# Kernel tuning notes

Hardware: AMD Instinct MI355X
Metric: run time of the kernel (lower is better)

Reference implementation:

```python
import jax, jax.numpy as jnp
import numpy as np

KH, KW, PAD, DIL, STRIDE = 3, 3, 1, 1, 1


def _conv2d(x, w):
    # plain dense conv, NCHW / OIHW, stride 1, pad 1
    return jax.lax.conv_general_dilated(
        x, w, window_strides=(STRIDE, STRIDE),
        padding=[(PAD, PAD), (PAD, PAD)],
        rhs_dilation=(DIL, DIL),
        dimension_numbers=('NCHW', 'OIHW', 'NCHW'))


def _deform_patches(x, offset):
    """Bilinear-sample deformable patches.
    x: [B,C,H,W], offset: [B,2K,Ho,Wo] with per-tap (dy,dx).
    Returns [B,C,K,Ho,Wo]."""
    B, C, H, W = x.shape
    Ho, Wo = offset.shape[2], offset.shape[3]
    K = KH * KW
    off = offset.reshape(B, K, 2, Ho, Wo)

    ky = jnp.repeat(jnp.arange(KH), KW)            # [K]
    kx = jnp.tile(jnp.arange(KW), KH)              # [K]
    base_y = (jnp.arange(Ho) * STRIDE - PAD)[None, :, None] + (DIL * ky)[:, None, None]  # [K,Ho,1]
    base_x = (jnp.arange(Wo) * STRIDE - PAD)[None, None, :] + (DIL * kx)[:, None, None]  # [K,1,Wo]

    sy = base_y[None].astype(x.dtype) + off[:, :, 0]   # [B,K,Ho,Wo]
    sx = base_x[None].astype(x.dtype) + off[:, :, 1]

    y0 = jnp.floor(sy); x0 = jnp.floor(sx)
    ly = sy - y0;       lx = sx - x0
    y0i = y0.astype(jnp.int32); x0i = x0.astype(jnp.int32)

    x_flat = x.reshape(B, C, H * W)

    def corner(yi, xi, wgt):
        valid = (yi >= 0) & (yi < H) & (xi >= 0) & (xi < W)   # zero padding outside
        idx = (jnp.clip(yi, 0, H - 1) * W + jnp.clip(xi, 0, W - 1))  # [B,K,Ho,Wo]
        gath = jax.vmap(lambda img, i: img[:, i.reshape(-1)])(x_flat, idx)  # [B,C,K*Ho*Wo]
        gath = gath.reshape(B, C, K, Ho, Wo)
        return gath * (wgt * valid.astype(x.dtype))[:, None]

    p = corner(y0i,     x0i,     (1 - ly) * (1 - lx))
    p = p + corner(y0i,     x0i + 1, (1 - ly) * lx)
    p = p + corner(y0i + 1, x0i,     ly * (1 - lx))
    p = p + corner(y0i + 1, x0i + 1, ly * lx)
    return p  # [B,C,K,Ho,Wo]


def setup_inputs() -> dict:
    key = jax.random.key(0)
    k1, k2, k3 = jax.random.split(key, 3)
    B, C, H, W = 8, 256, 64, 64
    Cout = 256
    x = jax.random.normal(k1, (B, C, H, W), dtype=jnp.float32)
    offset_w = jax.random.normal(k2, (2 * KH * KW, C, KH, KW), dtype=jnp.float32) * 0.02
    deform_w = jax.random.normal(k3, (Cout, C, KH, KW), dtype=jnp.float32) * 0.02
    return {"x": x, "offset_w": offset_w, "deform_w": deform_w}


def reference(x, offset_w, deform_w):
    # 1) offset-predicting conv
    offset = _conv2d(x, offset_w)                    # [B,2K,H,W]
    # 2) deformable conv = bilinear gather + contraction over (Cin, K)
    patches = _deform_patches(x, offset)             # [B,C,K,H,W]
    Cout = deform_w.shape[0]
    wk = deform_w.reshape(Cout, deform_w.shape[1], KH * KW)
    y = jnp.einsum('bckhw,ock->bohw', patches, wk)   # [B,Cout,H,W]
    # 3) avg + std channel attention (torch.std default: unbiased, ddof=1)
    avg = jnp.mean(y, axis=(2, 3), keepdims=True)
    std = jnp.std(y, axis=(2, 3), keepdims=True, ddof=1)
    attn = jax.nn.sigmoid(avg + std)
    return y * attn
```

## Files before the change

### kernel.cpp

```cpp
#include <hip/hip_runtime.h>
#include <hip/hip_bf16.h>
#include <math.h>

#define C_IN 256
#define H_   64
#define W_   64
#define B_   8
#define COUT 256
#define HW   (H_*W_)

typedef float f32x4 __attribute__((ext_vector_type(4)));
typedef short short8 __attribute__((ext_vector_type(8)));

static __device__ __forceinline__ int pack_bf16x2(float a, float b) {
    __hip_bfloat162 h = __float22bfloat162_rn(make_float2(a, b));
    union { __hip_bfloat162 h; int i; } u; u.h = h;
    return u.i;
}

static __device__ __forceinline__ void unpk(int v, float& lo, float& hi) {
    union { int i; float f; } a, b;
    a.i = v << 16;
    b.i = v & 0xffff0000;
    lo = a.f; hi = b.f;
}

__global__ __launch_bounds__(256) void prep_weights_kernel(
    const float* __restrict__ ow, const float* __restrict__ dw,
    short* __restrict__ wR, short* __restrict__ wO)
{
    int blk = blockIdx.x;
    int k   = blk / 288;
    int row = blk % 288;
    int c   = threadIdx.x;
    int cblk = c >> 6, ks = (c >> 5) & 1, q = (c >> 3) & 3, ce = c & 7;
    union { float f; unsigned u; } a;
    if (row < 256) {
        int o = row;
        a.f = dw[(size_t)o * 2304 + c * 9 + k];
        unsigned r = (a.u + 0x7fffu + ((a.u >> 16) & 1u)) >> 16;
        size_t idx = (size_t)(k * 8 + cblk * 2 + ks) * 8192
                   + (size_t)(o >> 4) * 512 + q * 128 + (o & 15) * 8 + ce;
        wR[idx] = (short)r;
    } else {
        int o = row - 256;
        a.f = (o < 18) ? ow[(size_t)o * 2304 + c * 9 + k] : 0.f;
        unsigned r = (a.u + 0x7fffu + ((a.u >> 16) & 1u)) >> 16;
        size_t idx = (size_t)(k * 8 + cblk * 2 + ks) * 1024
                   + (size_t)(o >> 4) * 512 + q * 128 + (o & 15) * 8 + ce;
        wO[idx] = (short)r;
    }
}

__global__ __launch_bounds__(256) void transpose_x_kernel(
    const float* __restrict__ x, unsigned short* __restrict__ xT)
{
    __shared__ float tile[64][257];
    const int tid = threadIdx.x;
    const int b = blockIdx.x >> 6, h = blockIdx.x & 63;
    const float* xb = x + ((size_t)b << 20) + h * 64;

#pragma unroll
    for (int pass = 0; pass < 16; ++pass) {
        int c  = pass * 16 + (tid >> 4);
        int w0 = (tid & 15) * 4;
        float4 v = *(const float4*)(xb + (size_t)c * 4096 + w0);
        tile[w0][c] = v.x; tile[w0 + 1][c] = v.y;
        tile[w0 + 2][c] = v.z; tile[w0 + 3][c] = v.w;
    }
    __syncthreads();

    int4* ob = (int4*)(xT + ((size_t)blockIdx.x << 14));
#pragma unroll
    for (int pass = 0; pass < 8; ++pass) {
        int idx = pass * 256 + tid;
        int w = idx >> 5, ch8 = idx & 31;
        const float* tr = &tile[w][ch8 * 8];
        int4 pk;
        pk.x = pack_bf16x2(tr[0], tr[1]);
        pk.y = pack_bf16x2(tr[2], tr[3]);
        pk.z = pack_bf16x2(tr[4], tr[5]);
        pk.w = pack_bf16x2(tr[6], tr[7]);
        ob[idx] = pk;
    }
}

__global__ __launch_bounds__(256, 2) void offset_mfma_kernel(
    const unsigned short* __restrict__ xT, const short* __restrict__ wO,
    float* __restrict__ offs)
{
    __shared__ int4 bT[2][64 * 8];

    const int tid = threadIdx.x;
    const int b   = blockIdx.x & 7;
    const int ho  = blockIdx.x >> 3;

    const int px = tid >> 2;
    const int cg = tid & 3;
    const int wv = tid >> 6;
    const int ln = tid & 63;
    const int lo = ln & 15;
    const int quad = ln >> 4;
    const int pxl = wv * 16 + lo;

    f32x4 acc[2];
    acc[0] = (f32x4){0.f, 0.f, 0.f, 0.f};
    acc[1] = (f32x4){0.f, 0.f, 0.f, 0.f};

    const unsigned short* xbb = xT + ((size_t)b << 20);
    const int4 zero4 = {0, 0, 0, 0};

    auto stageB = [&](int s, int buf) {
        int k = s >> 2, c0 = (s & 3) << 6;
        int yy = ho + k / 3 - 1;
        int xx = px + k % 3 - 1;
        bool valid = (yy >= 0) & (yy < 64) & (xx >= 0) & (xx < 64);
        int yc = min(max(yy, 0), 63), xc = min(max(xx, 0), 63);
        const int4* src = (const int4*)(xbb + (((size_t)yc * 64 + xc) << 8) + c0 + cg * 16);
        int4 p0 = valid ? src[0] : zero4;
        int4 p1 = valid ? src[1] : zero4;
        bT[buf][px * 8 + ((2 * cg)     ^ (px & 7))] = p0;
        bT[buf][px * 8 + ((2 * cg + 1) ^ (px & 7))] = p1;
    };

    stageB(0, 0);
    __syncthreads();

    for (int s = 0; s < 36; ++s) {
        const int cur = s & 1;
        if (s < 35) stageB(s + 1, cur ^ 1);

        const int k = s >> 2;
        const short* wkb = wO + (size_t)(k * 8 + (s & 3) * 2) * 1024 + ln * 8;
#pragma unroll
        for (int ks = 0; ks < 2; ++ks) {
            int ch = ks * 4 + quad;
            short8 bfr = *(const short8*)&bT[cur][pxl * 8 + (ch ^ (pxl & 7))];
#pragma unroll
            for (int t = 0; t < 2; ++t) {
                short8 afr = *(const short8*)(wkb + ks * 1024 + t * 512);
                acc[t] = __builtin_amdgcn_mfma_f32_16x16x32_bf16(afr, bfr, acc[t], 0, 0, 0);
            }
        }
        __syncthreads();
    }

#pragma unroll
    for (int t = 0; t < 2; ++t) {
#pragma unroll
        for (int r = 0; r < 4; ++r) {
            int o = t * 16 + quad * 4 + r;
            if (o < 18)
                offs[((size_t)b * 18 + o) * HW + ho * 64 + wv * 16 + lo] = acc[t][r];
        }
    }
}

__global__ __launch_bounds__(256, 4) void deform_mfma_kernel(
    const unsigned short* __restrict__ xT, const float* __restrict__ offs,
    const short* __restrict__ wR, float* __restrict__ y,
    float* __restrict__ sum_, float* __restrict__ sumsq_)
{
    __shared__ int4   meta_i[288];
    __shared__ float4 meta_w[288];
    __shared__ int4   bT[2][32 * 8];

    const int tid = threadIdx.x;
    const int b   = blockIdx.x & 7;
    const int ho  = (blockIdx.x >> 3) & 63;
    const int xh  = blockIdx.x >> 9;
    const int px0 = xh * 32;

    for (int e = tid; e < 288; e += 256) {
        int kk  = e >> 5;
        int pxe = px0 + (e & 31);
        float dy = offs[((size_t)b * 18 + 2 * kk)     * HW + ho * W_ + pxe];
        float dx = offs[((size_t)b * 18 + 2 * kk + 1) * HW + ho * W_ + pxe];
        float sy = (float)(ho - 1 + kk / 3) + dy;
        float sx = (float)(pxe - 1 + kk % 3) + dx;
        float y0f = floorf(sy), x0f = floorf(sx);
        float ly = sy - y0f, lx = sx - x0f;
        int y0 = (int)y0f, x0 = (int)x0f;
        int y1 = y0 + 1, x1 = x0 + 1;
        float wy0 = 1.f - ly, wx0 = 1.f - lx;
        bool vy0 = (y0 >= 0) & (y0 < H_), vy1 = (y1 >= 0) & (y1 < H_);
        bool vx0 = (x0 >= 0) & (x0 < W_), vx1 = (x1 >= 0) & (x1 < W_);
        int cy0 = min(max(y0, 0), H_ - 1), cy1 = min(max(y1, 0), H_ - 1);
        int cx0 = min(max(x0, 0), W_ - 1), cx1 = min(max(x1, 0), W_ - 1);
        int4 ii; float4 ww;
        ii.x = cy0 * W_ + cx0;  ww.x = wy0 * wx0 * ((vy0 & vx0) ? 1.f : 0.f);
        ii.y = cy0 * W_ + cx1;  ww.y = wy0 * lx  * ((vy0 & vx1) ? 1.f : 0.f);
        ii.z = cy1 * W_ + cx0;  ww.z = ly  * wx0 * ((vy1 & vx0) ? 1.f : 0.f);
        ii.w = cy1 * W_ + cx1;  ww.w = ly  * lx  * ((vy1 & vx1) ? 1.f : 0.f);
        meta_i[e] = ii;
        meta_w[e] = ww;
    }

    const int px = tid >> 3;
    const int cg = tid & 7;
    const int wv = tid >> 6;
    const int ln = tid & 63;
    const int lo = ln & 15;
    const int quad = ln >> 4;

    f32x4 acc[4][2];
#pragma unroll
    for (int t = 0; t < 4; ++t)
#pragma unroll
        for (int p = 0; p < 2; ++p)
            acc[t][p] = (f32x4){0.f, 0.f, 0.f, 0.f};

    const unsigned short* xbb = xT + ((size_t)b << 20) + cg * 8;

    int4 gA, gB, gC, gD;
    float4 ww;
    auto blend = [&](int av, int bv, int cv, int dv) -> int {
        float alo, ahi, blo, bhi, clo, chi, dlo, dhi;
        unpk(av, alo, ahi); unpk(bv, blo, bhi);
        unpk(cv, clo, chi); unpk(dv, dlo, dhi);
        float vlo = ww.x * alo + ww.y * blo + ww.z * clo + ww.w * dlo;
        float vhi = ww.x * ahi + ww.y * bhi + ww.z * chi + ww.w * dhi;
        return pack_bf16x2(vlo, vhi);
    };

    __syncthreads();

    {
        int4 ii = meta_i[px];
        ww = meta_w[px];
        gA = *(const int4*)(xbb + ((size_t)ii.x << 8));
        gB = *(const int4*)(xbb + ((size_t)ii.y << 8));
        gC = *(const int4*)(xbb + ((size_t)ii.z << 8));
        gD = *(const int4*)(xbb + ((size_t)ii.w << 8));
        int4 o0;
        o0.x = blend(gA.x, gB.x, gC.x, gD.x);
        o0.y = blend(gA.y, gB.y, gC.y, gD.y);
        o0.z = blend(gA.z, gB.z, gC.z, gD.z);
        o0.w = blend(gA.w, gB.w, gC.w, gD.w);
        bT[0][px * 8 + (cg ^ (px & 7))] = o0;
    }
    __syncthreads();

    for (int s = 0; s < 36; ++s) {
        const int cur = s & 1;
        const bool hasNext = (s < 35);

        if (hasNext) {
            int sn = s + 1;
            int kn = sn >> 2, cn = (sn & 3) << 6;
            int4 ii = meta_i[kn * 32 + px];
            ww = meta_w[kn * 32 + px];
            const unsigned short* xc = xbb + cn;
            gA = *(const int4*)(xc + ((size_t)ii.x << 8));
            gB = *(const int4*)(xc + ((size_t)ii.y << 8));
            gC = *(const int4*)(xc + ((size_t)ii.z << 8));
            gD = *(const int4*)(xc + ((size_t)ii.w << 8));
        }

        const int k = s >> 2;
        const short* wkb = wR + (size_t)(k * 8 + (s & 3) * 2) * 8192
                         + wv * 2048 + ln * 8;
#pragma unroll
        for (int ks = 0; ks < 2; ++ks) {
            int ch = ks * 4 + quad;
            short8 bfr[2];
#pragma unroll
            for (int p = 0; p < 2; ++p) {
                int pp = p * 16 + lo;
                bfr[p] = *(const short8*)&bT[cur][pp * 8 + (ch ^ (pp & 7))];
            }
#pragma unroll
            for (int t = 0; t < 4; ++t) {
                short8 afr = *(const short8*)(wkb + ks * 8192 + t * 512);
#pragma unroll
                for (int p = 0; p < 2; ++p)
                    acc[t][p] = __builtin_amdgcn_mfma_f32_16x16x32_bf16(
                        afr, bfr[p], acc[t][p], 0, 0, 0);
            }
        }

        if (hasNext) {
            int4 o0;
            o0.x = blend(gA.x, gB.x, gC.x, gD.x);
            o0.y = blend(gA.y, gB.y, gC.y, gD.y);
            o0.z = blend(gA.z, gB.z, gC.z, gD.z);
            o0.w = blend(gA.w, gB.w, gC.w, gD.w);
            bT[cur ^ 1][px * 8 + (cg ^ (px & 7))] = o0;
        }
        __syncthreads();
    }

    float* yb = y + ((size_t)b << 20) + ho * 64 + px0;
#pragma unroll
    for (int t = 0; t < 4; ++t) {
#pragma unroll
        for (int r = 0; r < 4; ++r) {
            int o = wv * 64 + t * 16 + quad * 4 + r;
            float sv = 0.f, qv = 0.f;
#pragma unroll
            for (int p = 0; p < 2; ++p) {
                float val = acc[t][p][r];
                yb[(size_t)o * HW + p * 16 + lo] = val;
                sv += val;
                qv += val * val;
            }
#pragma unroll
            for (int m = 1; m <= 8; m <<= 1) {
                sv += __shfl_xor(sv, m, 16);
                qv += __shfl_xor(qv, m, 16);
            }
            if (lo == 0) {
                atomicAdd(&sum_[b * COUT + o], sv);
                atomicAdd(&sumsq_[b * COUT + o], qv);
            }
        }
    }
}

__global__ __launch_bounds__(256) void attn_scale_kernel(
    const float* __restrict__ sum_, const float* __restrict__ sumsq_,
    float* __restrict__ y)
{
    int bo = blockIdx.x;
    float s = sum_[bo], q = sumsq_[bo];
    float mean = s * (1.f / 4096.f);
    float var  = (q - s * s * (1.f / 4096.f)) * (1.f / 4095.f);
    float sd   = sqrtf(fmaxf(var, 0.f));
    float attn = 1.f / (1.f + expf(-(mean + sd)));
    float4* yp = (float4*)(y + (size_t)bo * HW);
#pragma unroll
    for (int i = 0; i < 4; ++i) {
        float4 v = yp[threadIdx.x + i * 256];
        v.x *= attn; v.y *= attn; v.z *= attn; v.w *= attn;
        yp[threadIdx.x + i * 256] = v;
    }
}

extern "C" void kernel_launch(void* const* d_in, const int* in_sizes, int n_in,
                              void* d_out, int out_size, void* d_ws, size_t ws_size,
                              hipStream_t stream)
{
    const float* x  = (const float*)d_in[0];
    const float* ow = (const float*)d_in[1];
    const float* dw = (const float*)d_in[2];
    float* out = (float*)d_out;
    float* ws  = (float*)d_ws;

    float*          offs = ws;
    unsigned short* xT   = (unsigned short*)(ws + 589824);
    short*          wR   = (short*)(xT + 8388608);
    short*          wO   = wR + 589824;
    float*          sum_ = (float*)(wO + 73728);
    float*          sumsq_ = sum_ + 2048;

    hipMemsetAsync(sum_, 0, 2 * 2048 * sizeof(float), stream);

    prep_weights_kernel<<<9 * 288, 256, 0, stream>>>(ow, dw, wR, wO);
    transpose_x_kernel<<<512, 256, 0, stream>>>(x, xT);
    offset_mfma_kernel<<<512, 256, 0, stream>>>(xT, wO, offs);
    deform_mfma_kernel<<<1024, 256, 0, stream>>>(xT, offs, wR, out, sum_, sumsq_);
    attn_scale_kernel<<<2048, 256, 0, stream>>>(sum_, sumsq_, out);
}
```

Measured before the change: 200.6 us.

## Deepen gather prefetch to two stages and retile offset conv over half-rows

Both MFMA kernels now issue global loads two stages ahead, holding two register sets, so gather latency overlaps with more MFMA work. The offset conv kernel is retiled to 32-pixel half-rows over 1024 blocks, with each wave owning one output fragment, and its occupancy hint is raised. MFMA sections get raised wave priority, and the bilinear blend uses packed float2 math. The cost is higher register pressure from the extra in-flight loads, which could reduce occupancy.

```diff
diff --git a/kernel.cpp b/kernel.cpp
--- a/kernel.cpp
+++ b/kernel.cpp
@@ -10,6 +10,7 @@
 #define HW   (H_*W_)
 
 typedef float f32x4 __attribute__((ext_vector_type(4)));
+typedef float f32x2 __attribute__((ext_vector_type(2)));
 typedef short short8 __attribute__((ext_vector_type(8)));
 
 static __device__ __forceinline__ int pack_bf16x2(float a, float b) {
@@ -18,11 +19,12 @@
     return u.i;
 }
 
-static __device__ __forceinline__ void unpk(int v, float& lo, float& hi) {
+static __device__ __forceinline__ f32x2 up2(int v) {
     union { int i; float f; } a, b;
     a.i = v << 16;
     b.i = v & 0xffff0000;
-    lo = a.f; hi = b.f;
+    f32x2 r; r[0] = a.f; r[1] = b.f;
+    return r;
 }
 
 __global__ __launch_bounds__(256) void prep_weights_kernel(
@@ -85,74 +87,82 @@
     }
 }
 
-__global__ __launch_bounds__(256, 2) void offset_mfma_kernel(
+__global__ __launch_bounds__(256, 4) void offset_mfma_kernel(
     const unsigned short* __restrict__ xT, const short* __restrict__ wO,
     float* __restrict__ offs)
 {
-    __shared__ int4 bT[2][64 * 8];
+    __shared__ int4 bT[2][32 * 8];
 
     const int tid = threadIdx.x;
     const int b   = blockIdx.x & 7;
-    const int ho  = blockIdx.x >> 3;
-
-    const int px = tid >> 2;
-    const int cg = tid & 3;
+    const int ho  = (blockIdx.x >> 3) & 63;
+    const int xh  = blockIdx.x >> 9;
+    const int px0 = xh * 32;
+
+    const int px = tid >> 3;
+    const int cg = tid & 7;
     const int wv = tid >> 6;
     const int ln = tid & 63;
     const int lo = ln & 15;
     const int quad = ln >> 4;
-    const int pxl = wv * 16 + lo;
-
-    f32x4 acc[2];
-    acc[0] = (f32x4){0.f, 0.f, 0.f, 0.f};
-    acc[1] = (f32x4){0.f, 0.f, 0.f, 0.f};
+    const int tfrag = wv >> 1;
+    const int pfr   = wv & 1;
+    const int pxl   = pfr * 16 + lo;
+
+    f32x4 acc = (f32x4){0.f, 0.f, 0.f, 0.f};
 
     const unsigned short* xbb = xT + ((size_t)b << 20);
     const int4 zero4 = {0, 0, 0, 0};
 
-    auto stageB = [&](int s, int buf) {
+    auto issueO = [&](int s, int4& p) {
         int k = s >> 2, c0 = (s & 3) << 6;
         int yy = ho + k / 3 - 1;
-        int xx = px + k % 3 - 1;
+        int xx = px0 + px + k % 3 - 1;
+        int yc = min(max(yy, 0), 63), xc = min(max(xx, 0), 63);
+        p = *(const int4*)(xbb + (((size_t)yc * 64 + xc) << 8) + c0 + cg * 8);
+    };
+    auto writeB = [&](int s, int buf, const int4& p) {
+        int k = s >> 2;
+        int yy = ho + k / 3 - 1;
+        int xx = px0 + px + k % 3 - 1;
         bool valid = (yy >= 0) & (yy < 64) & (xx >= 0) & (xx < 64);
-        int yc = min(max(yy, 0), 63), xc = min(max(xx, 0), 63);
-        const int4* src = (const int4*)(xbb + (((size_t)yc * 64 + xc) << 8) + c0 + cg * 16);
-        int4 p0 = valid ? src[0] : zero4;
-        int4 p1 = valid ? src[1] : zero4;
-        bT[buf][px * 8 + ((2 * cg)     ^ (px & 7))] = p0;
-        bT[buf][px * 8 + ((2 * cg + 1) ^ (px & 7))] = p1;
-    };
-
-    stageB(0, 0);
-    __syncthreads();
-
-    for (int s = 0; s < 36; ++s) {
-        const int cur = s & 1;
-        if (s < 35) stageB(s + 1, cur ^ 1);
-
-        const int k = s >> 2;
-        const short* wkb = wO + (size_t)(k * 8 + (s & 3) * 2) * 1024 + ln * 8;
+        bT[buf][px * 8 + (cg ^ (px & 7))] = valid ? p : zero4;
+    };
+    auto mfmaO = [&](int s, int buf) {
+        int k = s >> 2;
+        const short* wkb = wO + (size_t)(k * 8 + (s & 3) * 2) * 1024
+                         + tfrag * 512 + ln * 8;
+        __builtin_amdgcn_s_setprio(1);
 #pragma unroll
         for (int ks = 0; ks < 2; ++ks) {
             int ch = ks * 4 + quad;
-            short8 bfr = *(const short8*)&bT[cur][pxl * 8 + (ch ^ (pxl & 7))];
-#pragma unroll
-            for (int t = 0; t < 2; ++t) {
-                short8 afr = *(const short8*)(wkb + ks * 1024 + t * 512);
-                acc[t] = __builtin_amdgcn_mfma_f32_16x16x32_bf16(afr, bfr, acc[t], 0, 0, 0);
-            }
+            short8 bfr = *(const short8*)&bT[buf][pxl * 8 + (ch ^ (pxl & 7))];
+            short8 afr = *(const short8*)(wkb + ks * 1024);
+            acc = __builtin_amdgcn_mfma_f32_16x16x32_bf16(afr, bfr, acc, 0, 0, 0);
         }
-        __syncthreads();
-    }
-
-#pragma unroll
-    for (int t = 0; t < 2; ++t) {
-#pragma unroll
-        for (int r = 0; r < 4; ++r) {
-            int o = t * 16 + quad * 4 + r;
-            if (o < 18)
-                offs[((size_t)b * 18 + o) * HW + ho * 64 + wv * 16 + lo] = acc[t][r];
-        }
+        __builtin_amdgcn_s_setprio(0);
+    };
+
+    int4 pa, pb;
+    issueO(0, pa);
+    issueO(1, pb);
+    writeB(0, 0, pa);
+    __syncthreads();
+
+#pragma unroll 1
+    for (int t = 0; t < 17; ++t) {
+        int s = 2 * t;
+        issueO(s + 2, pa); mfmaO(s, 0);     writeB(s + 1, 1, pb); __syncthreads();
+        issueO(s + 3, pb); mfmaO(s + 1, 1); writeB(s + 2, 0, pa); __syncthreads();
+    }
+    mfmaO(34, 0); writeB(35, 1, pb); __syncthreads();
+    mfmaO(35, 1);
+
+#pragma unroll
+    for (int r = 0; r < 4; ++r) {
+        int o = tfrag * 16 + quad * 4 + r;
+        if (o < 18)
+            offs[((size_t)b * 18 + o) * HW + ho * 64 + px0 + pfr * 16 + lo] = acc[r];
     }
 }
 
@@ -212,54 +222,36 @@
 
     const unsigned short* xbb = xT + ((size_t)b << 20) + cg * 8;
 
-    int4 gA, gB, gC, gD;
-    float4 ww;
-    auto blend = [&](int av, int bv, int cv, int dv) -> int {
-        float alo, ahi, blo, bhi, clo, chi, dlo, dhi;
-        unpk(av, alo, ahi); unpk(bv, blo, bhi);
-        unpk(cv, clo, chi); unpk(dv, dlo, dhi);
-        float vlo = ww.x * alo + ww.y * blo + ww.z * clo + ww.w * dlo;
-        float vhi = ww.x * ahi + ww.y * bhi + ww.z * chi + ww.w * dhi;
-        return pack_bf16x2(vlo, vhi);
-    };
-
-    __syncthreads();
-
-    {
-        int4 ii = meta_i[px];
-        ww = meta_w[px];
-        gA = *(const int4*)(xbb + ((size_t)ii.x << 8));
-        gB = *(const int4*)(xbb + ((size_t)ii.y << 8));
-        gC = *(const int4*)(xbb + ((size_t)ii.z << 8));
-        gD = *(const int4*)(xbb + ((size_t)ii.w << 8));
+    auto issueG = [&](int s, int4& gA, int4& gB, int4& gC, int4& gD) {
+        int kn = s >> 2, cn = (s & 3) << 6;
+        int4 ii = meta_i[kn * 32 + px];
+        const unsigned short* xc = xbb + cn;
+        gA = *(const int4*)(xc + ((size_t)ii.x << 8));
+        gB = *(const int4*)(xc + ((size_t)ii.y << 8));
+        gC = *(const int4*)(xc + ((size_t)ii.z << 8));
+        gD = *(const int4*)(xc + ((size_t)ii.w << 8));
+    };
+    auto blendW = [&](int s, int buf, const int4& gA, const int4& gB,
+                      const int4& gC, const int4& gD) {
+        int kn = s >> 2;
+        float4 w4 = meta_w[kn * 32 + px];
+        auto bl = [&](int av, int bv, int cv, int dv) -> int {
+            f32x2 r = up2(av) * w4.x + up2(bv) * w4.y
+                    + up2(cv) * w4.z + up2(dv) * w4.w;
+            return pack_bf16x2(r[0], r[1]);
+        };
         int4 o0;
-        o0.x = blend(gA.x, gB.x, gC.x, gD.x);
-        o0.y = blend(gA.y, gB.y, gC.y, gD.y);
-        o0.z = blend(gA.z, gB.z, gC.z, gD.z);
-        o0.w = blend(gA.w, gB.w, gC.w, gD.w);
-        bT[0][px * 8 + (cg ^ (px & 7))] = o0;
-    }
-    __syncthreads();
-
-    for (int s = 0; s < 36; ++s) {
-        const int cur = s & 1;
-        const bool hasNext = (s < 35);
-
-        if (hasNext) {
-            int sn = s + 1;
-            int kn = sn >> 2, cn = (sn & 3) << 6;
-            int4 ii = meta_i[kn * 32 + px];
-            ww = meta_w[kn * 32 + px];
-            const unsigned short* xc = xbb + cn;
-            gA = *(const int4*)(xc + ((size_t)ii.x << 8));
-            gB = *(const int4*)(xc + ((size_t)ii.y << 8));
-            gC = *(const int4*)(xc + ((size_t)ii.z << 8));
-            gD = *(const int4*)(xc + ((size_t)ii.w << 8));
-        }
-
+        o0.x = bl(gA.x, gB.x, gC.x, gD.x);
+        o0.y = bl(gA.y, gB.y, gC.y, gD.y);
+        o0.z = bl(gA.z, gB.z, gC.z, gD.z);
+        o0.w = bl(gA.w, gB.w, gC.w, gD.w);
+        bT[buf][px * 8 + (cg ^ (px & 7))] = o0;
+    };
+    auto mfmaStage = [&](int s, int buf) {
         const int k = s >> 2;
         const short* wkb = wR + (size_t)(k * 8 + (s & 3) * 2) * 8192
                          + wv * 2048 + ln * 8;
+        __builtin_amdgcn_s_setprio(1);
 #pragma unroll
         for (int ks = 0; ks < 2; ++ks) {
             int ch = ks * 4 + quad;
@@ -267,7 +259,7 @@
 #pragma unroll
             for (int p = 0; p < 2; ++p) {
                 int pp = p * 16 + lo;
-                bfr[p] = *(const short8*)&bT[cur][pp * 8 + (ch ^ (pp & 7))];
+                bfr[p] = *(const short8*)&bT[buf][pp * 8 + (ch ^ (pp & 7))];
             }
 #pragma unroll
             for (int t = 0; t < 4; ++t) {
@@ -278,17 +270,34 @@
                         afr, bfr[p], acc[t][p], 0, 0, 0);
             }
         }
-
-        if (hasNext) {
-            int4 o0;
-            o0.x = blend(gA.x, gB.x, gC.x, gD.x);
-            o0.y = blend(gA.y, gB.y, gC.y, gD.y);
-            o0.z = blend(gA.z, gB.z, gC.z, gD.z);
-            o0.w = blend(gA.w, gB.w, gC.w, gD.w);
-            bT[cur ^ 1][px * 8 + (cg ^ (px & 7))] = o0;
-        }
+        __builtin_amdgcn_s_setprio(0);
+    };
+
+    int4 a0, a1, a2, a3, b0, b1, b2, b3;
+
+    __syncthreads();
+
+    issueG(0, a0, a1, a2, a3);
+    issueG(1, b0, b1, b2, b3);
+    blendW(0, 0, a0, a1, a2, a3);
+    __syncthreads();
+
+#pragma unroll 1
+    for (int t = 0; t < 17; ++t) {
+        int s = 2 * t;
+        issueG(s + 2, a0, a1, a2, a3);
+        mfmaStage(s, 0);
+        blendW(s + 1, 1, b0, b1, b2, b3);
         __syncthreads();
-    }
+        issueG(s + 3, b0, b1, b2, b3);
+        mfmaStage(s + 1, 1);
+        blendW(s + 2, 0, a0, a1, a2, a3);
+        __syncthreads();
+    }
+    mfmaStage(34, 0);
+    blendW(35, 1, b0, b1, b2, b3);
+    __syncthreads();
+    mfmaStage(35, 1);
 
     float* yb = y + ((size_t)b << 20) + ho * 64 + px0;
 #pragma unroll
@@ -357,7 +366,7 @@
 
     prep_weights_kernel<<<9 * 288, 256, 0, stream>>>(ow, dw, wR, wO);
     transpose_x_kernel<<<512, 256, 0, stream>>>(x, xT);
-    offset_mfma_kernel<<<512, 256, 0, stream>>>(xT, wO, offs);
+    offset_mfma_kernel<<<1024, 256, 0, stream>>>(xT, wO, offs);
     deform_mfma_kernel<<<1024, 256, 0, stream>>>(xT, offs, wR, out, sum_, sumsq_);
     attn_scale_kernel<<<2048, 256, 0, stream>>>(sum_, sumsq_, out);
 }
```

Measured after the change: 256.6 us. +27.9%, slower.

## Widen deform tile to full row and deepen gather pipeline

Applied to the files above, without the earlier changes.

The deformable-conv kernel now gives each block a full 64-pixel output row instead of half a row, which halves the grid and doubles the MFMA N-tile, so every weight fragment loaded from global memory is reused across four pixel groups instead of two. The gather uses two register sets to keep loads two stages ahead of the MFMA stage, with each thread fetching 16 channels per corner. It also adds sched_barrier and setprio hints, and the blend uses packed f32x2 math. Register pressure goes up (launch bounds lowered to 2 blocks per SIMD), and the 512-block grid may underfill the GPU.

```diff
diff --git a/kernel.cpp b/kernel.cpp
--- a/kernel.cpp
+++ b/kernel.cpp
@@ -10,6 +10,7 @@
 #define HW   (H_*W_)
 
 typedef float f32x4 __attribute__((ext_vector_type(4)));
+typedef float f32x2 __attribute__((ext_vector_type(2)));
 typedef short short8 __attribute__((ext_vector_type(8)));
 
 static __device__ __forceinline__ int pack_bf16x2(float a, float b) {
@@ -18,11 +19,12 @@
     return u.i;
 }
 
-static __device__ __forceinline__ void unpk(int v, float& lo, float& hi) {
+static __device__ __forceinline__ f32x2 up2(int v) {
     union { int i; float f; } a, b;
     a.i = v << 16;
     b.i = v & 0xffff0000;
-    lo = a.f; hi = b.f;
+    f32x2 r; r[0] = a.f; r[1] = b.f;
+    return r;
 }
 
 __global__ __launch_bounds__(256) void prep_weights_kernel(
@@ -156,24 +158,22 @@
     }
 }
 
-__global__ __launch_bounds__(256, 4) void deform_mfma_kernel(
+__global__ __launch_bounds__(256, 2) void deform_mfma_kernel(
     const unsigned short* __restrict__ xT, const float* __restrict__ offs,
     const short* __restrict__ wR, float* __restrict__ y,
     float* __restrict__ sum_, float* __restrict__ sumsq_)
 {
-    __shared__ int4   meta_i[288];
-    __shared__ float4 meta_w[288];
-    __shared__ int4   bT[2][32 * 8];
+    __shared__ int4   meta_i[576];
+    __shared__ float4 meta_w[576];
+    __shared__ int4   bT[2][64 * 8];
 
     const int tid = threadIdx.x;
     const int b   = blockIdx.x & 7;
-    const int ho  = (blockIdx.x >> 3) & 63;
-    const int xh  = blockIdx.x >> 9;
-    const int px0 = xh * 32;
-
-    for (int e = tid; e < 288; e += 256) {
-        int kk  = e >> 5;
-        int pxe = px0 + (e & 31);
+    const int ho  = blockIdx.x >> 3;
+
+    for (int e = tid; e < 576; e += 256) {
+        int kk  = e >> 6;
+        int pxe = e & 63;
         float dy = offs[((size_t)b * 18 + 2 * kk)     * HW + ho * W_ + pxe];
         float dx = offs[((size_t)b * 18 + 2 * kk + 1) * HW + ho * W_ + pxe];
         float sy = (float)(ho - 1 + kk / 3) + dy;
@@ -196,101 +196,122 @@
         meta_w[e] = ww;
     }
 
-    const int px = tid >> 3;
-    const int cg = tid & 7;
+    const int px = tid >> 2;
+    const int cg = tid & 3;
     const int wv = tid >> 6;
     const int ln = tid & 63;
     const int lo = ln & 15;
     const int quad = ln >> 4;
 
-    f32x4 acc[4][2];
+    f32x4 acc[4][4];
 #pragma unroll
     for (int t = 0; t < 4; ++t)
 #pragma unroll
-        for (int p = 0; p < 2; ++p)
+        for (int p = 0; p < 4; ++p)
             acc[t][p] = (f32x4){0.f, 0.f, 0.f, 0.f};
 
-    const unsigned short* xbb = xT + ((size_t)b << 20) + cg * 8;
-
-    int4 gA, gB, gC, gD;
-    float4 ww;
-    auto blend = [&](int av, int bv, int cv, int dv) -> int {
-        float alo, ahi, blo, bhi, clo, chi, dlo, dhi;
-        unpk(av, alo, ahi); unpk(bv, blo, bhi);
-        unpk(cv, clo, chi); unpk(dv, dlo, dhi);
-        float vlo = ww.x * alo + ww.y * blo + ww.z * clo + ww.w * dlo;
-        float vhi = ww.x * ahi + ww.y * bhi + ww.z * chi + ww.w * dhi;
-        return pack_bf16x2(vlo, vhi);
-    };
-
-    __syncthreads();
-
-    {
-        int4 ii = meta_i[px];
-        ww = meta_w[px];
-        gA = *(const int4*)(xbb + ((size_t)ii.x << 8));
-        gB = *(const int4*)(xbb + ((size_t)ii.y << 8));
-        gC = *(const int4*)(xbb + ((size_t)ii.z << 8));
-        gD = *(const int4*)(xbb + ((size_t)ii.w << 8));
-        int4 o0;
-        o0.x = blend(gA.x, gB.x, gC.x, gD.x);
-        o0.y = blend(gA.y, gB.y, gC.y, gD.y);
-        o0.z = blend(gA.z, gB.z, gC.z, gD.z);
-        o0.w = blend(gA.w, gB.w, gC.w, gD.w);
-        bT[0][px * 8 + (cg ^ (px & 7))] = o0;
-    }
-    __syncthreads();
-
-    for (int s = 0; s < 36; ++s) {
-        const int cur = s & 1;
-        const bool hasNext = (s < 35);
-
-        if (hasNext) {
-            int sn = s + 1;
-            int kn = sn >> 2, cn = (sn & 3) << 6;
-            int4 ii = meta_i[kn * 32 + px];
-            ww = meta_w[kn * 32 + px];
-            const unsigned short* xc = xbb + cn;
-            gA = *(const int4*)(xc + ((size_t)ii.x << 8));
-            gB = *(const int4*)(xc + ((size_t)ii.y << 8));
-            gC = *(const int4*)(xc + ((size_t)ii.z << 8));
-            gD = *(const int4*)(xc + ((size_t)ii.w << 8));
-        }
-
+    const unsigned short* xbb = xT + ((size_t)b << 20) + cg * 16;
+
+#define ISSUE_G(S, G0,G1,G2,G3,G4,G5,G6,G7)                                   \
+    {                                                                         \
+        int kn_ = (S) >> 2, cn_ = ((S) & 3) << 6;                             \
+        int4 ii_ = meta_i[kn_ * 64 + px];                                     \
+        const unsigned short* xc_ = xbb + cn_;                                \
+        const int4* pA_ = (const int4*)(xc_ + ((size_t)ii_.x << 8));          \
+        const int4* pB_ = (const int4*)(xc_ + ((size_t)ii_.y << 8));          \
+        const int4* pC_ = (const int4*)(xc_ + ((size_t)ii_.z << 8));          \
+        const int4* pD_ = (const int4*)(xc_ + ((size_t)ii_.w << 8));          \
+        G0 = pA_[0]; G1 = pA_[1];                                             \
+        G2 = pB_[0]; G3 = pB_[1];                                             \
+        G4 = pC_[0]; G5 = pC_[1];                                             \
+        G6 = pD_[0]; G7 = pD_[1];                                             \
+    }
+
+#define BLEND_W(S, BUF, G0,G1,G2,G3,G4,G5,G6,G7)                              \
+    {                                                                         \
+        int kn_ = (S) >> 2;                                                   \
+        float4 w4_ = meta_w[kn_ * 64 + px];                                   \
+        auto bl_ = [&](int av, int bv, int cv, int dv) -> int {               \
+            f32x2 r_ = up2(av) * w4_.x + up2(bv) * w4_.y                      \
+                     + up2(cv) * w4_.z + up2(dv) * w4_.w;                     \
+            return pack_bf16x2(r_[0], r_[1]);                                 \
+        };                                                                    \
+        int4 o0_, o1_;                                                        \
+        o0_.x = bl_(G0.x, G2.x, G4.x, G6.x);                                  \
+        o0_.y = bl_(G0.y, G2.y, G4.y, G6.y);                                  \
+        o0_.z = bl_(G0.z, G2.z, G4.z, G6.z);                                  \
+        o0_.w = bl_(G0.w, G2.w, G4.w, G6.w);                                  \
+        o1_.x = bl_(G1.x, G3.x, G5.x, G7.x);                                  \
+        o1_.y = bl_(G1.y, G3.y, G5.y, G7.y);                                  \
+        o1_.z = bl_(G1.z, G3.z, G5.z, G7.z);                                  \
+        o1_.w = bl_(G1.w, G3.w, G5.w, G7.w);                                  \
+        bT[BUF][px * 8 + ((2 * cg)     ^ (px & 7))] = o0_;                    \
+        bT[BUF][px * 8 + ((2 * cg + 1) ^ (px & 7))] = o1_;                    \
+    }
+
+    auto mfmaStage = [&](int s, int buf) {
         const int k = s >> 2;
         const short* wkb = wR + (size_t)(k * 8 + (s & 3) * 2) * 8192
                          + wv * 2048 + ln * 8;
+        short8 afr[2][4];
+#pragma unroll
+        for (int ks = 0; ks < 2; ++ks)
+#pragma unroll
+            for (int t = 0; t < 4; ++t)
+                afr[ks][t] = *(const short8*)(wkb + ks * 8192 + t * 512);
+        __builtin_amdgcn_s_setprio(1);
 #pragma unroll
         for (int ks = 0; ks < 2; ++ks) {
             int ch = ks * 4 + quad;
-            short8 bfr[2];
-#pragma unroll
-            for (int p = 0; p < 2; ++p) {
+            short8 bfr[4];
+#pragma unroll
+            for (int p = 0; p < 4; ++p) {
                 int pp = p * 16 + lo;
-                bfr[p] = *(const short8*)&bT[cur][pp * 8 + (ch ^ (pp & 7))];
-            }
-#pragma unroll
-            for (int t = 0; t < 4; ++t) {
-                short8 afr = *(const short8*)(wkb + ks * 8192 + t * 512);
-#pragma unroll
-                for (int p = 0; p < 2; ++p)
+                bfr[p] = *(const short8*)&bT[buf][pp * 8 + (ch ^ (pp & 7))];
+            }
+#pragma unroll
+            for (int t = 0; t < 4; ++t)
+#pragma unroll
+                for (int p = 0; p < 4; ++p)
                     acc[t][p] = __builtin_amdgcn_mfma_f32_16x16x32_bf16(
-                        afr, bfr[p], acc[t][p], 0, 0, 0);
-            }
+                        afr[ks][t], bfr[p], acc[t][p], 0, 0, 0);
         }
-
-        if (hasNext) {
-            int4 o0;
-            o0.x = blend(gA.x, gB.x, gC.x, gD.x);
-            o0.y = blend(gA.y, gB.y, gC.y, gD.y);
-            o0.z = blend(gA.z, gB.z, gC.z, gD.z);
-            o0.w = blend(gA.w, gB.w, gC.w, gD.w);
-            bT[cur ^ 1][px * 8 + (cg ^ (px & 7))] = o0;
-        }
+        __builtin_amdgcn_s_setprio(0);
+    };
+
+    int4 a0, a1, a2, a3, a4, a5, a6, a7;
+    int4 b0, b1, b2, b3, b4, b5, b6, b7;
+
+    __syncthreads();
+
+    ISSUE_G(0, a0,a1,a2,a3,a4,a5,a6,a7);
+    ISSUE_G(1, b0,b1,b2,b3,b4,b5,b6,b7);
+    BLEND_W(0, 0, a0,a1,a2,a3,a4,a5,a6,a7);
+    __syncthreads();
+
+#pragma unroll 1
+    for (int t = 0; t < 17; ++t) {
+        int s = 2 * t;
+        ISSUE_G(s + 2, a0,a1,a2,a3,a4,a5,a6,a7);
+        __builtin_amdgcn_sched_barrier(0);
+        mfmaStage(s, 0);
+        BLEND_W(s + 1, 1, b0,b1,b2,b3,b4,b5,b6,b7);
         __syncthreads();
-    }
-
-    float* yb = y + ((size_t)b << 20) + ho * 64 + px0;
+        ISSUE_G(s + 3, b0,b1,b2,b3,b4,b5,b6,b7);
+        __builtin_amdgcn_sched_barrier(0);
+        mfmaStage(s + 1, 1);
+        BLEND_W(s + 2, 0, a0,a1,a2,a3,a4,a5,a6,a7);
+        __syncthreads();
+    }
+    mfmaStage(34, 0);
+    BLEND_W(35, 1, b0,b1,b2,b3,b4,b5,b6,b7);
+    __syncthreads();
+    mfmaStage(35, 1);
+
+#undef ISSUE_G
+#undef BLEND_W
+
+    float* yb = y + ((size_t)b << 20) + ho * 64;
 #pragma unroll
     for (int t = 0; t < 4; ++t) {
 #pragma unroll
@@ -298,7 +319,7 @@
             int o = wv * 64 + t * 16 + quad * 4 + r;
             float sv = 0.f, qv = 0.f;
 #pragma unroll
-            for (int p = 0; p < 2; ++p) {
+            for (int p = 0; p < 4; ++p) {
                 float val = acc[t][p][r];
                 yb[(size_t)o * HW + p * 16 + lo] = val;
                 sv += val;
@@ -358,6 +379,6 @@
     prep_weights_kernel<<<9 * 288, 256, 0, stream>>>(ow, dw, wR, wO);
     transpose_x_kernel<<<512, 256, 0, stream>>>(x, xT);
     offset_mfma_kernel<<<512, 256, 0, stream>>>(xT, wO, offs);
-    deform_mfma_kernel<<<1024, 256, 0, stream>>>(xT, offs, wR, out, sum_, sumsq_);
+    deform_mfma_kernel<<<512, 256, 0, stream>>>(xT, offs, wR, out, sum_, sumsq_);
     attn_scale_kernel<<<2048, 256, 0, stream>>>(sum_, sumsq_, out);
 }
```

Result: faster. 188.0 us (-6.2%).
